# Optimization experiments

Measured on AMD Instinct MI355X. Metric: run time of the kernel, lower is better.

The kernel has to match this reference:

```python
import jax, jax.numpy as jnp
import numpy as np

B, S, D, H = 4, 2048, 2048, 16
HD = D // H  # 128


def setup_inputs() -> dict:
    key = jax.random.key(0)
    k1, k2, k3 = jax.random.split(key, 3)
    sc = 1.0 / np.sqrt(D)
    return {
        "x": jax.random.normal(k1, (B, S, D), dtype=jnp.float32),
        "W_qkv": jax.random.normal(k2, (D, 3 * D), dtype=jnp.float32) * sc,
        "W_out": jax.random.normal(k3, (D, D), dtype=jnp.float32) * sc,
        "b_out": jnp.zeros((D,), dtype=jnp.float32),
    }


def _rotate_half(t):
    t1, t2 = jnp.split(t, 2, axis=-1)
    return jnp.concatenate([-t2, t1], axis=-1)


def reference(x, W_qkv, W_out, b_out):
    b, s, d = x.shape
    qkv = jnp.einsum('bsd,de->bse', x, W_qkv)  # fused QKV projection
    q, k, v = jnp.split(qkv, 3, axis=-1)
    # [b, h, s, hd]
    q = q.reshape(b, s, H, HD).transpose(0, 2, 1, 3)
    k = k.reshape(b, s, H, HD).transpose(0, 2, 1, 3)
    v = v.reshape(b, s, H, HD).transpose(0, 2, 1, 3)
    # RoPE (NeoX-style half-split), past_kv=None so positions = arange(s)
    pos = jnp.arange(s, dtype=jnp.float32)
    theta = 1.0 / (10000.0 ** (jnp.arange(0, HD, 2, dtype=jnp.float32) / HD))
    angles = pos[:, None] * theta[None, :]           # [s, hd/2]
    cos = jnp.concatenate([jnp.cos(angles)] * 2, -1)  # [s, hd] (repeat halves)
    sin = jnp.concatenate([jnp.sin(angles)] * 2, -1)
    cos = cos[None, None]  # [1,1,s,hd]
    sin = sin[None, None]
    q = q * cos + _rotate_half(q) * sin
    k = k * cos + _rotate_half(k) * sin
    # causal SDPA, scale = 1/sqrt(head_dim)
    scale = 1.0 / jnp.sqrt(jnp.asarray(HD, dtype=q.dtype))
    scores = jnp.einsum('bhqd,bhkd->bhqk', q, k) * scale
    causal = jnp.tril(jnp.ones((s, s), dtype=bool))
    scores = jnp.where(causal[None, None], scores, jnp.finfo(scores.dtype).min)
    attn = jax.nn.softmax(scores, axis=-1)
    out = jnp.einsum('bhqk,bhkd->bhqd', attn, v)
    out = out.transpose(0, 2, 1, 3).reshape(b, s, D)
    return jnp.einsum('bsd,de->bse', out, W_out) + b_out
```

## Files before the change

### kernel.cpp

```cpp
#include <hip/hip_runtime.h>

typedef unsigned short ushort_t;
typedef unsigned int u32;
typedef __attribute__((ext_vector_type(8))) short bf16x8;
typedef __attribute__((ext_vector_type(8))) unsigned short u16x8;
typedef __attribute__((ext_vector_type(4))) float f32x4;

#define B_ 4
#define S_ 2048
#define D_ 2048
#define H_ 16
#define HD_ 128

__device__ __forceinline__ ushort_t f2bf(float f) {
  u32 x = __builtin_bit_cast(u32, f);
  x += 0x7fffu + ((x >> 16) & 1u);
  return (ushort_t)(x >> 16);
}
__device__ __forceinline__ float bf2f(ushort_t u) {
  u32 x = ((u32)u) << 16;
  return __builtin_bit_cast(float, x);
}

#define GLL16(srcp, ldsp)                                            \
  __builtin_amdgcn_global_load_lds(                                  \
      (const __attribute__((address_space(1))) u32*)(srcp),          \
      (__attribute__((address_space(3))) u32*)(ldsp), 16, 0, 0)

struct __align__(8) us4 { ushort_t x, y, z, w; };

__global__ void k_cvt_bf16(const float* __restrict__ in, ushort_t* __restrict__ out, int n) {
  int i = (blockIdx.x * 256 + threadIdx.x) * 4;
  if (i >= n) return;
  float4 v = *(const float4*)(in + i);
  us4 o;
  o.x = f2bf(v.x); o.y = f2bf(v.y); o.z = f2bf(v.z); o.w = f2bf(v.w);
  *(us4*)(out + i) = o;
}

__global__ void k_transpose_bf16(const float* __restrict__ in, ushort_t* __restrict__ out,
                                 int R, int C) {
  __shared__ float ld[32][33];
  int c0 = blockIdx.x * 32, r0 = blockIdx.y * 32;
  int tc = threadIdx.x & 31, tr = threadIdx.x >> 5;
#pragma unroll
  for (int i = 0; i < 4; ++i) {
    int r = tr + i * 8;
    ld[r][tc] = in[(size_t)(r0 + r) * C + c0 + tc];
  }
  __syncthreads();
#pragma unroll
  for (int i = 0; i < 4; ++i) {
    int r = tr + i * 8;
    out[(size_t)(c0 + r) * R + r0 + tc] = f2bf(ld[tc][r]);
  }
}

__global__ void k_rope_tables(float* __restrict__ cost, float* __restrict__ sint) {
  int i = blockIdx.x * 256 + threadIdx.x;
  int s = i >> 6, j = i & 63;
  double th = pow(10000.0, -(double)j / 64.0);
  double a = (double)s * th;
  cost[i] = (float)cos(a);
  sint[i] = (float)sin(a);
}

template <int FINAL>
__global__ __launch_bounds__(512) void k_gemm8p(const ushort_t* __restrict__ A,
                                                const ushort_t* __restrict__ Bt,
                                                void* __restrict__ Cout,
                                                const float* __restrict__ bias,
                                                int M, int N, int K) {
  __shared__ __attribute__((aligned(16))) ushort_t As[2][256 * 64];
  __shared__ __attribute__((aligned(16))) ushort_t Bs[2][256 * 64];
  const int tid = threadIdx.x;
  const int w = tid >> 6, l = tid & 63;
  const int lr = l & 15, lg = l >> 4;

  const int cpx = gridDim.x >> 3;
  const int bid = blockIdx.x;
  const int swzid = (bid & 7) * cpx + (bid >> 3);
  const int nbn = N >> 8;
  const size_t m0 = (size_t)(swzid / nbn) * 256;
  const size_t n0 = (size_t)(swzid % nbn) * 256;

  const size_t Kp = (size_t)K * 2;
  const char* Ab = (const char*)A + m0 * Kp;
  const char* Bb = (const char*)Bt + n0 * Kp;

  const int r0 = tid >> 3;
  const int ci16 = (tid & 7) * 16;
  const int sw0 = (((tid & 7) ^ (r0 & 7)) << 4);

#define STG_HALF(gbase, hrow, ldsbase, tcol)                                   \
  {                                                                            \
    GLL16((gbase) + (size_t)((hrow) + r0) * Kp + (tcol) + sw0,                 \
          (char*)(ldsbase) + ((hrow) + r0) * 128 + ci16);                      \
    GLL16((gbase) + (size_t)((hrow) + r0 + 64) * Kp + (tcol) + sw0,            \
          (char*)(ldsbase) + ((hrow) + r0 + 64) * 128 + ci16);                 \
  }

  const int cko0 = (((0 * 4 + lg) ^ (lr & 7)) << 4);
  const int cko1 = (((1 * 4 + lg) ^ (lr & 7)) << 4);

  f32x4 acc[16][2] = {};
  const int NT = K >> 6;

  STG_HALF(Ab, 0, As[0], 0);
  STG_HALF(Bb, 0, Bs[0], 0);
  STG_HALF(Bb, 128, Bs[0], 0);
  STG_HALF(Ab, 128, As[0], 0);
  if (w < 4) asm volatile("s_waitcnt vmcnt(4)");
  else       asm volatile("s_waitcnt vmcnt(2)");
  __builtin_amdgcn_sched_barrier(0);
  __builtin_amdgcn_s_barrier();

  bf16x8 bq[2][2];
  for (int t = 0; t < NT; ++t) {
    const int buf = t & 1;
    const char* Ac = (const char*)As[buf];
    const char* Bc = (const char*)Bs[buf];
    const size_t tc1 = (size_t)(t + 1) * 128;
    const bool more = (t + 1 < NT);
#pragma unroll
    for (int p = 0; p < 4; ++p) {
      if (more) {
        if (p == 0) STG_HALF(Ab, 0, As[buf ^ 1], tc1)
        else if (p == 1) STG_HALF(Bb, 0, Bs[buf ^ 1], tc1)
        else if (p == 2) STG_HALF(Bb, 128, Bs[buf ^ 1], tc1)
        else STG_HALF(Ab, 128, As[buf ^ 1], tc1)
      }
      bf16x8 af[4][2];
#pragma unroll
      for (int m = 0; m < 4; ++m) {
        const int row = p * 64 + m * 16 + lr;
        af[m][0] = *(const bf16x8*)(Ac + row * 128 + cko0);
        af[m][1] = *(const bf16x8*)(Ac + row * 128 + cko1);
      }
      if (p == 0) {
#pragma unroll
        for (int n = 0; n < 2; ++n) {
          const int row = w * 32 + n * 16 + lr;
          bq[n][0] = *(const bf16x8*)(Bc + row * 128 + cko0);
          bq[n][1] = *(const bf16x8*)(Bc + row * 128 + cko1);
        }
      }
      __builtin_amdgcn_s_barrier();
      asm volatile("s_waitcnt lgkmcnt(0)");
      __builtin_amdgcn_sched_barrier(0);
      __builtin_amdgcn_s_setprio(1);
#pragma unroll
      for (int m = 0; m < 4; ++m)
#pragma unroll
        for (int n = 0; n < 2; ++n) {
          acc[p * 4 + m][n] =
              __builtin_amdgcn_mfma_f32_16x16x32_bf16(af[m][0], bq[n][0], acc[p * 4 + m][n], 0, 0, 0);
          acc[p * 4 + m][n] =
              __builtin_amdgcn_mfma_f32_16x16x32_bf16(af[m][1], bq[n][1], acc[p * 4 + m][n], 0, 0, 0);
        }
      __builtin_amdgcn_s_setprio(0);
      if (p == 1) {
        if (more) asm volatile("s_waitcnt vmcnt(4)");
        else      asm volatile("s_waitcnt vmcnt(0)");
        __builtin_amdgcn_sched_barrier(0);
      } else if (p == 3 && more) {
        if (w < 4) asm volatile("s_waitcnt vmcnt(4)");
        else       asm volatile("s_waitcnt vmcnt(2)");
        __builtin_amdgcn_sched_barrier(0);
      }
      __builtin_amdgcn_s_barrier();
    }
  }

#pragma unroll
  for (int n = 0; n < 2; ++n) {
    const size_t col = n0 + w * 32 + n * 16 + lr;
    float bia = FINAL ? bias[col] : 0.f;
#pragma unroll
    for (int mq = 0; mq < 16; ++mq) {
#pragma unroll
      for (int j = 0; j < 4; ++j) {
        const size_t row = m0 + mq * 16 + lg * 4 + j;
        if (FINAL) ((float*)Cout)[row * N + col] = acc[mq][n][j] + bia;
        else       ((ushort_t*)Cout)[row * N + col] = f2bf(acc[mq][n][j]);
      }
    }
  }
#undef STG_HALF
}

__global__ void k_split_rope(const ushort_t* __restrict__ tmp, ushort_t* __restrict__ dst,
                             const float* __restrict__ cost, const float* __restrict__ sint,
                             int mode, float qscale) {
  int s0 = blockIdx.x * 32;
  int h = blockIdx.y;
  int b = blockIdx.z;
  int bh = b * H_ + h;
  if (mode < 2) {
    const int t = threadIdx.x;
    const int sr = t >> 3, dj = (t & 7) * 8;
    const int s = s0 + sr;
    const size_t base = (size_t)(b * S_ + s) * D_ + h * HD_;
    u16x8 lo = *(const u16x8*)(tmp + base + dj);
    u16x8 hi = *(const u16x8*)(tmp + base + 64 + dj);
    const float* cs = cost + s * 64 + dj;
    const float* sn = sint + s * 64 + dj;
    u16x8 olo, ohi;
#pragma unroll
    for (int j = 0; j < 8; ++j) {
      float fl = bf2f(lo[j]), fh = bf2f(hi[j]);
      float c = cs[j], sv = sn[j];
      olo[j] = f2bf((fl * c - fh * sv) * qscale);
      ohi[j] = f2bf((fh * c + fl * sv) * qscale);
    }
    ushort_t* dp = dst + ((size_t)bh * S_ + s) * HD_;
    *(u16x8*)(dp + dj) = olo;
    *(u16x8*)(dp + 64 + dj) = ohi;
  } else {
    __shared__ ushort_t ld[32][132];
#pragma unroll
    for (int i = 0; i < 2; ++i) {
      int e = i * 256 + threadIdx.x;
      int sr = e >> 4, dj = (e & 15) * 8;
      *(u16x8*)&ld[sr][dj] = *(const u16x8*)(tmp + (size_t)(b * S_ + s0 + sr) * D_ + h * HD_ + dj);
    }
    __syncthreads();
#pragma unroll
    for (int i = 0; i < 16; ++i) {
      int e = i * 256 + threadIdx.x;
      int d = e >> 5, sr = e & 31;
      dst[((size_t)bh * HD_ + d) * S_ + s0 + sr] = ld[sr][d];
    }
  }
}

__global__ __launch_bounds__(256, 2) void k_attn4(const ushort_t* __restrict__ Q,
                                                  const ushort_t* __restrict__ K,
                                                  const ushort_t* __restrict__ Vt,
                                                  ushort_t* __restrict__ O) {
  __shared__ __attribute__((aligned(16))) ushort_t Ks[2][64 * 128];
  __shared__ __attribute__((aligned(16))) ushort_t Vs[128 * 64];
  __shared__ __attribute__((aligned(16))) ushort_t Pl[8][16 * 72];

  const int id = blockIdx.x;
  const int work = (id & 7) * 128 + (id >> 3);
  const int bh = work >> 4;
  const int qt = 15 - (work & 15);
  const int b = bh >> 4, h = bh & 15;

  const int tid = threadIdx.x;
  const int w = tid >> 6, l = tid & 63;
  const int lr = l & 15, lg = l >> 4;
  const int qb = qt * 128 + w * 32;

  const ushort_t* Qp = Q + (size_t)bh * S_ * HD_;
  const char* Kpb = (const char*)(K + (size_t)bh * S_ * HD_);
  const char* Vpb = (const char*)(Vt + (size_t)bh * HD_ * S_);

  int kr[4], ksz[4], vr[4], vsz[4];
#pragma unroll
  for (int r = 0; r < 4; ++r) {
    int c = r * 256 + tid;
    kr[r] = c >> 4;
    ksz[r] = (((c & 15) ^ (kr[r] & 15)) << 4);
    vr[r] = c >> 3;
    vsz[r] = (((c & 7) ^ (vr[r] & 7)) << 4);
  }

#define STAGE_K(kb_, bufi)                                                       \
  {                                                                              \
    _Pragma("unroll") for (int r = 0; r < 4; ++r)                                \
        GLL16(Kpb + (size_t)((kb_) + kr[r]) * 256 + ksz[r],                      \
              (char*)Ks[bufi] + (size_t)(r * 256 + tid) * 16);                   \
  }
#define STAGE_V(kb_)                                                             \
  {                                                                              \
    _Pragma("unroll") for (int r = 0; r < 4; ++r)                                \
        GLL16(Vpb + (size_t)vr[r] * (S_ * 2) + (size_t)(kb_) * 2 + vsz[r],       \
              (char*)Vs + (size_t)(r * 256 + tid) * 16);                         \
  }

  bf16x8 qf[2][4];
#pragma unroll
  for (int f = 0; f < 2; ++f)
#pragma unroll
    for (int dw = 0; dw < 4; ++dw)
      qf[f][dw] = *(const bf16x8*)(Qp + (size_t)(qb + f * 16 + lr) * HD_ + dw * 32 + lg * 8);

  f32x4 oacc[2][8] = {};
  float mr[2] = {-1e30f, -1e30f};
  float lsum[2] = {0.f, 0.f};
  const int nkt = 2 * qt + 2;

  STAGE_K(0, 0);
  for (int kt = 0; kt < nkt; ++kt) {
    const int kb = kt * 64;
    const int cur = kt & 1;
    const bool morek = (kt + 1 < nkt);
    if (morek) STAGE_K(kb + 64, cur ^ 1);
    STAGE_V(kb);
    if (morek) asm volatile("s_waitcnt vmcnt(8)");
    else       asm volatile("s_waitcnt vmcnt(4)");
    __builtin_amdgcn_sched_barrier(0);
    __builtin_amdgcn_s_barrier();

    const bool live = (kb <= qb + 31);
    f32x4 st[2][4];
    if (live) {
      const char* Kc = (const char*)Ks[cur];
      __builtin_amdgcn_s_setprio(1);
#pragma unroll
      for (int t = 0; t < 4; ++t) {
        bf16x8 kf[4];
#pragma unroll
        for (int dw = 0; dw < 4; ++dw)
          kf[dw] = *(const bf16x8*)(Kc + (t * 16 + lr) * 256 + (((dw * 4 + lg) ^ lr) << 4));
        f32x4 a0 = {}, a1 = {};
#pragma unroll
        for (int dw = 0; dw < 4; ++dw) {
          a0 = __builtin_amdgcn_mfma_f32_16x16x32_bf16(kf[dw], qf[0][dw], a0, 0, 0, 0);
          a1 = __builtin_amdgcn_mfma_f32_16x16x32_bf16(kf[dw], qf[1][dw], a1, 0, 0, 0);
        }
        st[0][t] = a0;
        st[1][t] = a1;
      }
      __builtin_amdgcn_s_setprio(0);

#pragma unroll
      for (int f = 0; f < 2; ++f) {
        const int qg = qb + f * 16 + lr;
        const bool full = (kb + 63) <= (qb + f * 16);
        float tmax = -1e30f;
        if (full) {
#pragma unroll
          for (int t = 0; t < 4; ++t)
#pragma unroll
            for (int j = 0; j < 4; ++j) tmax = fmaxf(tmax, st[f][t][j]);
        } else {
#pragma unroll
          for (int t = 0; t < 4; ++t)
#pragma unroll
            for (int j = 0; j < 4; ++j) {
              int kg = kb + t * 16 + lg * 4 + j;
              float s = (kg > qg) ? -1e30f : st[f][t][j];
              st[f][t][j] = s;
              tmax = fmaxf(tmax, s);
            }
        }
        tmax = fmaxf(tmax, __shfl_xor(tmax, 16, 64));
        tmax = fmaxf(tmax, __shfl_xor(tmax, 32, 64));
        if (!__all(tmax <= mr[f] + 8.f)) {
          float mnew = fmaxf(mr[f], tmax);
          float alpha = exp2f(mr[f] - mnew);
          mr[f] = mnew;
          lsum[f] *= alpha;
          float a0 = __shfl(alpha, lg * 4 + 0, 64);
          float a1 = __shfl(alpha, lg * 4 + 1, 64);
          float a2 = __shfl(alpha, lg * 4 + 2, 64);
          float a3 = __shfl(alpha, lg * 4 + 3, 64);
#pragma unroll
          for (int dt = 0; dt < 8; ++dt) {
            oacc[f][dt][0] *= a0;
            oacc[f][dt][1] *= a1;
            oacc[f][dt][2] *= a2;
            oacc[f][dt][3] *= a3;
          }
        }
        float psum = 0.f;
        ushort_t* Pw = (ushort_t*)Pl[w * 2 + f];
#pragma unroll
        for (int t = 0; t < 4; ++t) {
          float p0 = exp2f(st[f][t][0] - mr[f]);
          float p1 = exp2f(st[f][t][1] - mr[f]);
          float p2 = exp2f(st[f][t][2] - mr[f]);
          float p3 = exp2f(st[f][t][3] - mr[f]);
          psum += (p0 + p1) + (p2 + p3);
          u32 pk0, pk1;
          asm("v_cvt_pk_bf16_f32 %0, %1, %2" : "=v"(pk0) : "v"(p0), "v"(p1));
          asm("v_cvt_pk_bf16_f32 %0, %1, %2" : "=v"(pk1) : "v"(p2), "v"(p3));
          *(u32*)&Pw[lr * 72 + t * 16 + lg * 4] = pk0;
          *(u32*)&Pw[lr * 72 + t * 16 + lg * 4 + 2] = pk1;
        }
        psum += __shfl_xor(psum, 16, 64);
        psum += __shfl_xor(psum, 32, 64);
        lsum[f] += psum;
      }
    }
    if (morek) asm volatile("s_waitcnt vmcnt(4)");
    else       asm volatile("s_waitcnt vmcnt(0)");
    __builtin_amdgcn_sched_barrier(0);
    __builtin_amdgcn_s_barrier();

    if (live) {
      __builtin_amdgcn_s_setprio(1);
#pragma unroll
      for (int kw = 0; kw < 2; ++kw) {
        bf16x8 pa0 = *(const bf16x8*)&Pl[w * 2 + 0][lr * 72 + kw * 32 + lg * 8];
        bf16x8 pa1 = *(const bf16x8*)&Pl[w * 2 + 1][lr * 72 + kw * 32 + lg * 8];
#pragma unroll
        for (int dt = 0; dt < 8; ++dt) {
          bf16x8 vf = *(const bf16x8*)((const char*)Vs + (dt * 16 + lr) * 128 +
                                       (((kw * 4 + lg) ^ (lr & 7)) << 4));
          oacc[0][dt] = __builtin_amdgcn_mfma_f32_16x16x32_bf16(pa0, vf, oacc[0][dt], 0, 0, 0);
          oacc[1][dt] = __builtin_amdgcn_mfma_f32_16x16x32_bf16(pa1, vf, oacc[1][dt], 0, 0, 0);
        }
      }
      __builtin_amdgcn_s_setprio(0);
    }
    __builtin_amdgcn_s_barrier();
  }

#pragma unroll
  for (int f = 0; f < 2; ++f) {
    float l0 = __shfl(lsum[f], lg * 4 + 0, 64);
    float l1 = __shfl(lsum[f], lg * 4 + 1, 64);
    float l2 = __shfl(lsum[f], lg * 4 + 2, 64);
    float l3 = __shfl(lsum[f], lg * 4 + 3, 64);
    float i0 = 1.f / l0, i1 = 1.f / l1, i2 = 1.f / l2, i3 = 1.f / l3;
    ushort_t* Op = O + (size_t)(b * S_ + qb + f * 16) * D_ + h * HD_;
#pragma unroll
    for (int dt = 0; dt < 8; ++dt) {
      Op[(size_t)(lg * 4 + 0) * D_ + dt * 16 + lr] = f2bf(oacc[f][dt][0] * i0);
      Op[(size_t)(lg * 4 + 1) * D_ + dt * 16 + lr] = f2bf(oacc[f][dt][1] * i1);
      Op[(size_t)(lg * 4 + 2) * D_ + dt * 16 + lr] = f2bf(oacc[f][dt][2] * i2);
      Op[(size_t)(lg * 4 + 3) * D_ + dt * 16 + lr] = f2bf(oacc[f][dt][3] * i3);
    }
  }
#undef STAGE_K
#undef STAGE_V
}

extern "C" void kernel_launch(void* const* d_in, const int* in_sizes, int n_in,
                              void* d_out, int out_size, void* d_ws, size_t ws_size,
                              hipStream_t stream) {
  const float* x = (const float*)d_in[0];
  const float* Wqkv = (const float*)d_in[1];
  const float* Wout = (const float*)d_in[2];
  const float* bout = (const float*)d_in[3];
  char* ws = (char*)d_ws;

  ushort_t* xb = (ushort_t*)(ws + 0);
  ushort_t* Wqt = (ushort_t*)(ws + 33554432ull);
  ushort_t* tmp = (ushort_t*)(ws + 58720256ull);
  ushort_t* Qb = (ushort_t*)(ws + 92274688ull);
  ushort_t* Kb = (ushort_t*)(ws + 125829120ull);
  ushort_t* Vb = (ushort_t*)(ws + 159383552ull);
  float* cost = (float*)(ws + 192937984ull);
  float* sint = (float*)(ws + 193462272ull);

  const int M = B_ * S_;
  const float kSc = 0.08838834764831845f * 1.4426950408889634f;

  k_cvt_bf16<<<dim3((M * D_) / 4 / 256), 256, 0, stream>>>(x, xb, M * D_);
  k_transpose_bf16<<<dim3(3 * D_ / 32, D_ / 32), 256, 0, stream>>>(Wqkv, Wqt, D_, 3 * D_);
  k_rope_tables<<<dim3(S_ * 64 / 256), 256, 0, stream>>>(cost, sint);

  for (int p = 0; p < 3; ++p) {
    k_gemm8p<0><<<dim3((M / 256) * (D_ / 256)), 512, 0, stream>>>(
        xb, Wqt + (size_t)p * D_ * D_, tmp, nullptr, M, D_, D_);
    ushort_t* dst = (p == 0) ? Qb : (p == 1) ? Kb : Vb;
    k_split_rope<<<dim3(S_ / 32, H_, B_), 256, 0, stream>>>(
        tmp, dst, cost, sint, p, (p == 0) ? kSc : 1.0f);
  }

  k_attn4<<<dim3((S_ / 128) * B_ * H_), 256, 0, stream>>>(Qb, Kb, Vb, xb );

  k_transpose_bf16<<<dim3(D_ / 32, D_ / 32), 256, 0, stream>>>(Wout, tmp, D_, D_);
  k_gemm8p<1><<<dim3((M / 256) * (D_ / 256)), 512, 0, stream>>>(
      xb, tmp, d_out, bout, M, D_, D_);
}
```

Measured before the change: 554.4 us.

## Fuse QKV GEMMs, scatter heads in epilogue, restructure GEMM warps and attention V loads

The three per-projection GEMMs become one fused QKV GEMM whose epilogue writes straight into per-head [b,h,s,d] layout, so the separate split kernel and the tmp round trip go away. RoPE now runs in place, and V gets its own transpose kernel. The GEMM moves to a 2x4 warp grid with 128x64 warp tiles, different load staging and fewer barriers, at 2 blocks per CU. Attention drops the LDS staging of V in favour of direct global loads, swizzles the P buffer and raises occupancy to 3 blocks. The risks are register pressure and uncoalesced global V reads.

```diff
diff --git a/kernel.cpp b/kernel.cpp
--- a/kernel.cpp
+++ b/kernel.cpp
@@ -65,17 +65,21 @@
   sint[i] = (float)sin(a);
 }
 
-template <int FINAL>
-__global__ __launch_bounds__(512) void k_gemm8p(const ushort_t* __restrict__ A,
-                                                const ushort_t* __restrict__ Bt,
-                                                void* __restrict__ Cout,
-                                                const float* __restrict__ bias,
-                                                int M, int N, int K) {
+template <int MODE>
+__global__ __launch_bounds__(512, 2) void k_gemm8w(const ushort_t* __restrict__ A,
+                                                   const ushort_t* __restrict__ Bt,
+                                                   void* __restrict__ Cout,
+                                                   const float* __restrict__ bias,
+                                                   int M, int N, int K) {
   __shared__ __attribute__((aligned(16))) ushort_t As[2][256 * 64];
   __shared__ __attribute__((aligned(16))) ushort_t Bs[2][256 * 64];
   const int tid = threadIdx.x;
   const int w = tid >> 6, l = tid & 63;
   const int lr = l & 15, lg = l >> 4;
+  const int wm = w >> 2, wn = w & 3;
+  const int ga = w & 3;
+  const int hbB = wn >> 1;
+  const int rbB = (w & 1) | ((w >> 1) & 2);
 
   const int cpx = gridDim.x >> 3;
   const int bid = blockIdx.x;
@@ -88,164 +92,196 @@
   const char* Ab = (const char*)A + m0 * Kp;
   const char* Bb = (const char*)Bt + n0 * Kp;
 
-  const int r0 = tid >> 3;
-  const int ci16 = (tid & 7) * 16;
-  const int sw0 = (((tid & 7) ^ (r0 & 7)) << 4);
-
-#define STG_HALF(gbase, hrow, ldsbase, tcol)                                   \
-  {                                                                            \
-    GLL16((gbase) + (size_t)((hrow) + r0) * Kp + (tcol) + sw0,                 \
-          (char*)(ldsbase) + ((hrow) + r0) * 128 + ci16);                      \
-    GLL16((gbase) + (size_t)((hrow) + r0 + 64) * Kp + (tcol) + sw0,            \
-          (char*)(ldsbase) + ((hrow) + r0 + 64) * 128 + ci16);                 \
-  }
-
-  const int cko0 = (((0 * 4 + lg) ^ (lr & 7)) << 4);
-  const int cko1 = (((1 * 4 + lg) ^ (lr & 7)) << 4);
-
-  f32x4 acc[16][2] = {};
+  int arow[4], acs[4], adst[4], brow[4], bcs[4], bdst[4];
+#pragma unroll
+  for (int j = 0; j < 4; ++j) {
+    int c = j * 64 + l;
+    int ra = wm * 128 + ga * 32 + (c >> 3);
+    arow[j] = ra;
+    acs[j] = ((c & 7) ^ (ra & 7)) << 4;
+    adst[j] = ra * 128 + ((c & 7) << 4);
+    int rb = hbB * 128 + rbB * 32 + (c >> 3);
+    brow[j] = rb;
+    bcs[j] = ((c & 7) ^ (rb & 7)) << 4;
+    bdst[j] = rb * 128 + ((c & 7) << 4);
+  }
+
+#define STG_A(colb, bufi)                                                  \
+  { _Pragma("unroll") for (int j = 0; j < 4; ++j)                          \
+      GLL16(Ab + (size_t)arow[j] * Kp + (colb) + acs[j],                   \
+            (char*)As[bufi] + adst[j]); }
+#define STG_B(colb, bufi)                                                  \
+  { _Pragma("unroll") for (int j = 0; j < 4; ++j)                          \
+      GLL16(Bb + (size_t)brow[j] * Kp + (colb) + bcs[j],                   \
+            (char*)Bs[bufi] + bdst[j]); }
+
+  f32x4 acc[8][4] = {};
   const int NT = K >> 6;
 
-  STG_HALF(Ab, 0, As[0], 0);
-  STG_HALF(Bb, 0, Bs[0], 0);
-  STG_HALF(Bb, 128, Bs[0], 0);
-  STG_HALF(Ab, 128, As[0], 0);
-  if (w < 4) asm volatile("s_waitcnt vmcnt(4)");
-  else       asm volatile("s_waitcnt vmcnt(2)");
-  __builtin_amdgcn_sched_barrier(0);
-  __builtin_amdgcn_s_barrier();
-
-  bf16x8 bq[2][2];
+  STG_B((size_t)0, 0);
+  STG_A((size_t)0, 0);
+
   for (int t = 0; t < NT; ++t) {
     const int buf = t & 1;
     const char* Ac = (const char*)As[buf];
     const char* Bc = (const char*)Bs[buf];
-    const size_t tc1 = (size_t)(t + 1) * 128;
     const bool more = (t + 1 < NT);
+    const size_t tcol = (size_t)(t + 1) * 128;
+    bf16x8 bq[4][2];
 #pragma unroll
     for (int p = 0; p < 4; ++p) {
-      if (more) {
-        if (p == 0) STG_HALF(Ab, 0, As[buf ^ 1], tc1)
-        else if (p == 1) STG_HALF(Bb, 0, Bs[buf ^ 1], tc1)
-        else if (p == 2) STG_HALF(Bb, 128, Bs[buf ^ 1], tc1)
-        else STG_HALF(Ab, 128, As[buf ^ 1], tc1)
-      }
-      bf16x8 af[4][2];
-#pragma unroll
-      for (int m = 0; m < 4; ++m) {
-        const int row = p * 64 + m * 16 + lr;
-        af[m][0] = *(const bf16x8*)(Ac + row * 128 + cko0);
-        af[m][1] = *(const bf16x8*)(Ac + row * 128 + cko1);
-      }
       if (p == 0) {
-#pragma unroll
-        for (int n = 0; n < 2; ++n) {
-          const int row = w * 32 + n * 16 + lr;
-          bq[n][0] = *(const bf16x8*)(Bc + row * 128 + cko0);
-          bq[n][1] = *(const bf16x8*)(Bc + row * 128 + cko1);
+        if (ga == 0) asm volatile("s_waitcnt vmcnt(0)");
+        else         asm volatile("s_waitcnt vmcnt(4)");
+        __builtin_amdgcn_sched_barrier(0);
+      } else if (p == 1) {
+        if (ga == 1) {
+          if (more) asm volatile("s_waitcnt vmcnt(4)");
+          else      asm volatile("s_waitcnt vmcnt(0)");
+          __builtin_amdgcn_sched_barrier(0);
+        }
+      } else if (p == 2) {
+        if (ga == 2) {
+          if (more) asm volatile("s_waitcnt vmcnt(4)");
+          else      asm volatile("s_waitcnt vmcnt(0)");
+          __builtin_amdgcn_sched_barrier(0);
+        }
+      } else {
+        if (ga == 3) {
+          if (more) asm volatile("s_waitcnt vmcnt(8)");
+          else      asm volatile("s_waitcnt vmcnt(0)");
+          __builtin_amdgcn_sched_barrier(0);
         }
       }
       __builtin_amdgcn_s_barrier();
+      if (p == 0 && more) {
+        STG_B(tcol, buf ^ 1);
+        if (ga == 0) STG_A(tcol, buf ^ 1);
+      }
+      if (p == 2 && more && ga != 0) STG_A(tcol, buf ^ 1);
+      bf16x8 af[2][2];
+#pragma unroll
+      for (int m2 = 0; m2 < 2; ++m2) {
+        const int row = wm * 128 + (p * 2 + m2) * 16 + lr;
+#pragma unroll
+        for (int k2 = 0; k2 < 2; ++k2)
+          af[m2][k2] = *(const bf16x8*)(Ac + row * 128 + (((k2 * 4 + lg) ^ (lr & 7)) << 4));
+      }
+      if (p == 0) {
+#pragma unroll
+        for (int n = 0; n < 4; ++n) {
+          const int row = wn * 64 + n * 16 + lr;
+#pragma unroll
+          for (int k2 = 0; k2 < 2; ++k2)
+            bq[n][k2] = *(const bf16x8*)(Bc + row * 128 + (((k2 * 4 + lg) ^ (lr & 7)) << 4));
+        }
+      }
       asm volatile("s_waitcnt lgkmcnt(0)");
       __builtin_amdgcn_sched_barrier(0);
       __builtin_amdgcn_s_setprio(1);
 #pragma unroll
-      for (int m = 0; m < 4; ++m)
-#pragma unroll
-        for (int n = 0; n < 2; ++n) {
-          acc[p * 4 + m][n] =
-              __builtin_amdgcn_mfma_f32_16x16x32_bf16(af[m][0], bq[n][0], acc[p * 4 + m][n], 0, 0, 0);
-          acc[p * 4 + m][n] =
-              __builtin_amdgcn_mfma_f32_16x16x32_bf16(af[m][1], bq[n][1], acc[p * 4 + m][n], 0, 0, 0);
+      for (int m2 = 0; m2 < 2; ++m2)
+#pragma unroll
+        for (int n = 0; n < 4; ++n) {
+          acc[p * 2 + m2][n] =
+              __builtin_amdgcn_mfma_f32_16x16x32_bf16(af[m2][0], bq[n][0], acc[p * 2 + m2][n], 0, 0, 0);
+          acc[p * 2 + m2][n] =
+              __builtin_amdgcn_mfma_f32_16x16x32_bf16(af[m2][1], bq[n][1], acc[p * 2 + m2][n], 0, 0, 0);
         }
       __builtin_amdgcn_s_setprio(0);
-      if (p == 1) {
-        if (more) asm volatile("s_waitcnt vmcnt(4)");
-        else      asm volatile("s_waitcnt vmcnt(0)");
-        __builtin_amdgcn_sched_barrier(0);
-      } else if (p == 3 && more) {
-        if (w < 4) asm volatile("s_waitcnt vmcnt(4)");
-        else       asm volatile("s_waitcnt vmcnt(2)");
-        __builtin_amdgcn_sched_barrier(0);
-      }
-      __builtin_amdgcn_s_barrier();
     }
   }
 
-#pragma unroll
-  for (int n = 0; n < 2; ++n) {
-    const size_t col = n0 + w * 32 + n * 16 + lr;
-    float bia = FINAL ? bias[col] : 0.f;
-#pragma unroll
-    for (int mq = 0; mq < 16; ++mq) {
-#pragma unroll
-      for (int j = 0; j < 4; ++j) {
-        const size_t row = m0 + mq * 16 + lg * 4 + j;
-        if (FINAL) ((float*)Cout)[row * N + col] = acc[mq][n][j] + bia;
-        else       ((ushort_t*)Cout)[row * N + col] = f2bf(acc[mq][n][j]);
-      }
+  if (MODE == 2) {
+#pragma unroll
+    for (int n = 0; n < 4; ++n) {
+      const size_t col = n0 + wn * 64 + n * 16 + lr;
+      const float bia = bias[col];
+#pragma unroll
+      for (int m = 0; m < 8; ++m)
+#pragma unroll
+        for (int j = 0; j < 4; ++j) {
+          const size_t row = m0 + wm * 128 + m * 16 + lg * 4 + j;
+          ((float*)Cout)[row * N + col] = acc[m][n][j] + bia;
+        }
     }
-  }
-#undef STG_HALF
-}
-
-__global__ void k_split_rope(const ushort_t* __restrict__ tmp, ushort_t* __restrict__ dst,
-                             const float* __restrict__ cost, const float* __restrict__ sint,
-                             int mode, float qscale) {
-  int s0 = blockIdx.x * 32;
-  int h = blockIdx.y;
-  int b = blockIdx.z;
+  } else {
+    ushort_t* Qbase = (ushort_t*)Cout;
+#pragma unroll
+    for (int n = 0; n < 4; ++n) {
+      const int col = (int)n0 + wn * 64 + n * 16 + lr;
+      const int p3 = col >> 11, rem = col & 2047;
+      const int h = rem >> 7, d = rem & 127;
+      ushort_t* base = Qbase + (size_t)p3 * 16777216ull + (size_t)h * (S_ * HD_) + d;
+#pragma unroll
+      for (int m = 0; m < 8; ++m)
+#pragma unroll
+        for (int j = 0; j < 4; ++j) {
+          const int row = (int)m0 + wm * 128 + m * 16 + lg * 4 + j;
+          const int b2 = row >> 11, s = row & 2047;
+          base[(size_t)b2 * (H_ * S_ * HD_) + (size_t)s * HD_] = f2bf(acc[m][n][j]);
+        }
+    }
+  }
+#undef STG_A
+#undef STG_B
+}
+
+__global__ void k_rope2(ushort_t* __restrict__ t8, const float* __restrict__ cost,
+                        const float* __restrict__ sint, float qscale) {
+  int s0 = blockIdx.x * 32, h = blockIdx.y, b = blockIdx.z;
   int bh = b * H_ + h;
-  if (mode < 2) {
-    const int t = threadIdx.x;
-    const int sr = t >> 3, dj = (t & 7) * 8;
-    const int s = s0 + sr;
-    const size_t base = (size_t)(b * S_ + s) * D_ + h * HD_;
-    u16x8 lo = *(const u16x8*)(tmp + base + dj);
-    u16x8 hi = *(const u16x8*)(tmp + base + 64 + dj);
-    const float* cs = cost + s * 64 + dj;
-    const float* sn = sint + s * 64 + dj;
-    u16x8 olo, ohi;
-#pragma unroll
-    for (int j = 0; j < 8; ++j) {
-      float fl = bf2f(lo[j]), fh = bf2f(hi[j]);
-      float c = cs[j], sv = sn[j];
-      olo[j] = f2bf((fl * c - fh * sv) * qscale);
-      ohi[j] = f2bf((fh * c + fl * sv) * qscale);
-    }
-    ushort_t* dp = dst + ((size_t)bh * S_ + s) * HD_;
-    *(u16x8*)(dp + dj) = olo;
-    *(u16x8*)(dp + 64 + dj) = ohi;
-  } else {
-    __shared__ ushort_t ld[32][132];
-#pragma unroll
-    for (int i = 0; i < 2; ++i) {
-      int e = i * 256 + threadIdx.x;
-      int sr = e >> 4, dj = (e & 15) * 8;
-      *(u16x8*)&ld[sr][dj] = *(const u16x8*)(tmp + (size_t)(b * S_ + s0 + sr) * D_ + h * HD_ + dj);
-    }
-    __syncthreads();
-#pragma unroll
-    for (int i = 0; i < 16; ++i) {
-      int e = i * 256 + threadIdx.x;
-      int d = e >> 5, sr = e & 31;
-      dst[((size_t)bh * HD_ + d) * S_ + s0 + sr] = ld[sr][d];
-    }
-  }
-}
-
-__global__ __launch_bounds__(256, 2) void k_attn4(const ushort_t* __restrict__ Q,
+  const int t = threadIdx.x;
+  const int sr = t >> 3, dj = (t & 7) * 8;
+  const int s = s0 + sr;
+  ushort_t* base = t8 + ((size_t)bh * S_ + s) * HD_;
+  u16x8 lo = *(const u16x8*)(base + dj);
+  u16x8 hi = *(const u16x8*)(base + 64 + dj);
+  const float* cs = cost + s * 64 + dj;
+  const float* sn = sint + s * 64 + dj;
+  u16x8 olo, ohi;
+#pragma unroll
+  for (int j = 0; j < 8; ++j) {
+    float fl = bf2f(lo[j]), fh = bf2f(hi[j]);
+    float c = cs[j], sv = sn[j];
+    olo[j] = f2bf((fl * c - fh * sv) * qscale);
+    ohi[j] = f2bf((fh * c + fl * sv) * qscale);
+  }
+  *(u16x8*)(base + dj) = olo;
+  *(u16x8*)(base + 64 + dj) = ohi;
+}
+
+__global__ void k_transT(const ushort_t* __restrict__ src, ushort_t* __restrict__ dst) {
+  __shared__ ushort_t ld[32][33];
+  int s0 = blockIdx.x * 32, d0 = blockIdx.y * 32, bh = blockIdx.z;
+  const ushort_t* S = src + (size_t)bh * S_ * HD_;
+  ushort_t* D = dst + (size_t)bh * HD_ * S_;
+  const int tid = threadIdx.x;
+#pragma unroll
+  for (int i = 0; i < 4; ++i) {
+    int e = i * 256 + tid;
+    int sr = e >> 5, dc = e & 31;
+    ld[sr][dc] = S[(size_t)(s0 + sr) * HD_ + d0 + dc];
+  }
+  __syncthreads();
+#pragma unroll
+  for (int i = 0; i < 4; ++i) {
+    int e = i * 256 + tid;
+    int dc = e >> 5, sr = e & 31;
+    D[(size_t)(d0 + dc) * S_ + s0 + sr] = ld[sr][dc];
+  }
+}
+
+__global__ __launch_bounds__(256, 3) void k_attn5(const ushort_t* __restrict__ Q,
                                                   const ushort_t* __restrict__ K,
                                                   const ushort_t* __restrict__ Vt,
                                                   ushort_t* __restrict__ O) {
   __shared__ __attribute__((aligned(16))) ushort_t Ks[2][64 * 128];
-  __shared__ __attribute__((aligned(16))) ushort_t Vs[128 * 64];
-  __shared__ __attribute__((aligned(16))) ushort_t Pl[8][16 * 72];
+  __shared__ __attribute__((aligned(16))) ushort_t Pl[8][1024];
 
   const int id = blockIdx.x;
-  const int work = (id & 7) * 128 + (id >> 3);
-  const int bh = work >> 4;
-  const int qt = 15 - (work & 15);
+  const int qt = 15 - (id >> 6);
+  const int bh = id & 63;
   const int b = bh >> 4, h = bh & 15;
 
   const int tid = threadIdx.x;
@@ -257,28 +293,20 @@
   const char* Kpb = (const char*)(K + (size_t)bh * S_ * HD_);
   const char* Vpb = (const char*)(Vt + (size_t)bh * HD_ * S_);
 
-  int kr[4], ksz[4], vr[4], vsz[4];
+  int kr[4], ksz[4];
 #pragma unroll
   for (int r = 0; r < 4; ++r) {
     int c = r * 256 + tid;
     kr[r] = c >> 4;
-    ksz[r] = (((c & 15) ^ (kr[r] & 15)) << 4);
-    vr[r] = c >> 3;
-    vsz[r] = (((c & 7) ^ (vr[r] & 7)) << 4);
+    ksz[r] = ((c & 15) ^ (kr[r] & 15)) << 4;
   }
 
 #define STAGE_K(kb_, bufi)                                                       \
-  {                                                                              \
-    _Pragma("unroll") for (int r = 0; r < 4; ++r)                                \
-        GLL16(Kpb + (size_t)((kb_) + kr[r]) * 256 + ksz[r],                      \
-              (char*)Ks[bufi] + (size_t)(r * 256 + tid) * 16);                   \
-  }
-#define STAGE_V(kb_)                                                             \
-  {                                                                              \
-    _Pragma("unroll") for (int r = 0; r < 4; ++r)                                \
-        GLL16(Vpb + (size_t)vr[r] * (S_ * 2) + (size_t)(kb_) * 2 + vsz[r],       \
-              (char*)Vs + (size_t)(r * 256 + tid) * 16);                         \
-  }
+  { _Pragma("unroll") for (int r = 0; r < 4; ++r)                                \
+      GLL16(Kpb + (size_t)((kb_) + kr[r]) * 256 + ksz[r],                        \
+            (char*)Ks[bufi] + (size_t)(r * 256 + tid) * 16); }
+
+  STAGE_K(0, 0);
 
   bf16x8 qf[2][4];
 #pragma unroll
@@ -292,22 +320,23 @@
   float lsum[2] = {0.f, 0.f};
   const int nkt = 2 * qt + 2;
 
-  STAGE_K(0, 0);
   for (int kt = 0; kt < nkt; ++kt) {
     const int kb = kt * 64;
     const int cur = kt & 1;
     const bool morek = (kt + 1 < nkt);
-    if (morek) STAGE_K(kb + 64, cur ^ 1);
-    STAGE_V(kb);
-    if (morek) asm volatile("s_waitcnt vmcnt(8)");
-    else       asm volatile("s_waitcnt vmcnt(4)");
+    if (morek) {
+      STAGE_K(kb + 64, cur ^ 1);
+      asm volatile("s_waitcnt vmcnt(4)");
+    } else {
+      asm volatile("s_waitcnt vmcnt(0)");
+    }
     __builtin_amdgcn_sched_barrier(0);
     __builtin_amdgcn_s_barrier();
 
     const bool live = (kb <= qb + 31);
-    f32x4 st[2][4];
     if (live) {
       const char* Kc = (const char*)Ks[cur];
+      f32x4 st[2][4];
       __builtin_amdgcn_s_setprio(1);
 #pragma unroll
       for (int t = 0; t < 4; ++t) {
@@ -367,7 +396,7 @@
           }
         }
         float psum = 0.f;
-        ushort_t* Pw = (ushort_t*)Pl[w * 2 + f];
+        char* Pw = (char*)Pl + (w * 2 + f) * 2048;
 #pragma unroll
         for (int t = 0; t < 4; ++t) {
           float p0 = exp2f(st[f][t][0] - mr[f]);
@@ -378,34 +407,35 @@
           u32 pk0, pk1;
           asm("v_cvt_pk_bf16_f32 %0, %1, %2" : "=v"(pk0) : "v"(p0), "v"(p1));
           asm("v_cvt_pk_bf16_f32 %0, %1, %2" : "=v"(pk1) : "v"(p2), "v"(p3));
-          *(u32*)&Pw[lr * 72 + t * 16 + lg * 4] = pk0;
-          *(u32*)&Pw[lr * 72 + t * 16 + lg * 4 + 2] = pk1;
+          const int byt = lr * 128 + (((2 * t + (lg >> 1)) ^ (lr & 7)) << 4) + ((lg & 1) << 3);
+          *(u32*)(Pw + byt) = pk0;
+          *(u32*)(Pw + byt + 4) = pk1;
         }
         psum += __shfl_xor(psum, 16, 64);
         psum += __shfl_xor(psum, 32, 64);
         lsum[f] += psum;
       }
-    }
-    if (morek) asm volatile("s_waitcnt vmcnt(4)");
-    else       asm volatile("s_waitcnt vmcnt(0)");
-    __builtin_amdgcn_sched_barrier(0);
-    __builtin_amdgcn_s_barrier();
-
-    if (live) {
-      __builtin_amdgcn_s_setprio(1);
+
+      const char* Pw0 = (const char*)Pl + (w * 2) * 2048;
+      const char* Pw1 = (const char*)Pl + (w * 2 + 1) * 2048;
 #pragma unroll
       for (int kw = 0; kw < 2; ++kw) {
-        bf16x8 pa0 = *(const bf16x8*)&Pl[w * 2 + 0][lr * 72 + kw * 32 + lg * 8];
-        bf16x8 pa1 = *(const bf16x8*)&Pl[w * 2 + 1][lr * 72 + kw * 32 + lg * 8];
+        bf16x8 vf[8];
+#pragma unroll
+        for (int dt = 0; dt < 8; ++dt)
+          vf[dt] = *(const bf16x8*)(Vpb + ((size_t)(dt * 16 + lr) * S_ + kb + kw * 32 + lg * 8) * 2);
+        const int pbyt = lr * 128 + (((kw * 4 + lg) ^ (lr & 7)) << 4);
+        bf16x8 pa0 = *(const bf16x8*)(Pw0 + pbyt);
+        bf16x8 pa1 = *(const bf16x8*)(Pw1 + pbyt);
+        __builtin_amdgcn_s_setprio(1);
 #pragma unroll
         for (int dt = 0; dt < 8; ++dt) {
-          bf16x8 vf = *(const bf16x8*)((const char*)Vs + (dt * 16 + lr) * 128 +
-                                       (((kw * 4 + lg) ^ (lr & 7)) << 4));
-          oacc[0][dt] = __builtin_amdgcn_mfma_f32_16x16x32_bf16(pa0, vf, oacc[0][dt], 0, 0, 0);
-          oacc[1][dt] = __builtin_amdgcn_mfma_f32_16x16x32_bf16(pa1, vf, oacc[1][dt], 0, 0, 0);
-        }
-      }
-      __builtin_amdgcn_s_setprio(0);
+          oacc[0][dt] = __builtin_amdgcn_mfma_f32_16x16x32_bf16(pa0, vf[dt], oacc[0][dt], 0, 0, 0);
+          oacc[1][dt] = __builtin_amdgcn_mfma_f32_16x16x32_bf16(pa1, vf[dt], oacc[1][dt], 0, 0, 0);
+        }
+        __builtin_amdgcn_s_setprio(0);
+        __builtin_amdgcn_sched_barrier(0);
+      }
     }
     __builtin_amdgcn_s_barrier();
   }
@@ -427,7 +457,6 @@
     }
   }
 #undef STAGE_K
-#undef STAGE_V
 }
 
 extern "C" void kernel_launch(void* const* d_in, const int* in_sizes, int n_in,
@@ -439,14 +468,14 @@
   const float* bout = (const float*)d_in[3];
   char* ws = (char*)d_ws;
 
-  ushort_t* xb = (ushort_t*)(ws + 0);
+  ushort_t* xb  = (ushort_t*)(ws + 0);
   ushort_t* Wqt = (ushort_t*)(ws + 33554432ull);
-  ushort_t* tmp = (ushort_t*)(ws + 58720256ull);
-  ushort_t* Qb = (ushort_t*)(ws + 92274688ull);
-  ushort_t* Kb = (ushort_t*)(ws + 125829120ull);
-  ushort_t* Vb = (ushort_t*)(ws + 159383552ull);
-  float* cost = (float*)(ws + 192937984ull);
-  float* sint = (float*)(ws + 193462272ull);
+  ushort_t* Qr  = (ushort_t*)(ws + 58720256ull);
+  ushort_t* Kr  = (ushort_t*)(ws + 92274688ull);
+  ushort_t* Vr  = (ushort_t*)(ws + 125829120ull);
+  ushort_t* Vt  = (ushort_t*)(ws + 159383552ull);
+  float* cost   = (float*)(ws + 192937984ull);
+  float* sint   = (float*)(ws + 193462272ull);
 
   const int M = B_ * S_;
   const float kSc = 0.08838834764831845f * 1.4426950408889634f;
@@ -455,17 +484,17 @@
   k_transpose_bf16<<<dim3(3 * D_ / 32, D_ / 32), 256, 0, stream>>>(Wqkv, Wqt, D_, 3 * D_);
   k_rope_tables<<<dim3(S_ * 64 / 256), 256, 0, stream>>>(cost, sint);
 
-  for (int p = 0; p < 3; ++p) {
-    k_gemm8p<0><<<dim3((M / 256) * (D_ / 256)), 512, 0, stream>>>(
-        xb, Wqt + (size_t)p * D_ * D_, tmp, nullptr, M, D_, D_);
-    ushort_t* dst = (p == 0) ? Qb : (p == 1) ? Kb : Vb;
-    k_split_rope<<<dim3(S_ / 32, H_, B_), 256, 0, stream>>>(
-        tmp, dst, cost, sint, p, (p == 0) ? kSc : 1.0f);
-  }
-
-  k_attn4<<<dim3((S_ / 128) * B_ * H_), 256, 0, stream>>>(Qb, Kb, Vb, xb );
-
-  k_transpose_bf16<<<dim3(D_ / 32, D_ / 32), 256, 0, stream>>>(Wout, tmp, D_, D_);
-  k_gemm8p<1><<<dim3((M / 256) * (D_ / 256)), 512, 0, stream>>>(
-      xb, tmp, d_out, bout, M, D_, D_);
-}
+  k_gemm8w<1><<<dim3((M / 256) * (3 * D_ / 256)), 512, 0, stream>>>(
+      xb, Wqt, Qr, nullptr, M, 3 * D_, D_);
+
+  k_rope2<<<dim3(S_ / 32, H_, B_), 256, 0, stream>>>(Qr, cost, sint, kSc);
+  k_rope2<<<dim3(S_ / 32, H_, B_), 256, 0, stream>>>(Kr, cost, sint, 1.0f);
+  k_transT<<<dim3(S_ / 32, HD_ / 32, B_ * H_), 256, 0, stream>>>(Vr, Vt);
+
+  k_transpose_bf16<<<dim3(D_ / 32, D_ / 32), 256, 0, stream>>>(Wout, Vr, D_, D_);
+
+  k_attn5<<<dim3((S_ / 128) * B_ * H_), 256, 0, stream>>>(Qr, Kr, Vt, xb );
+
+  k_gemm8w<2><<<dim3((M / 256) * (D_ / 256)), 512, 0, stream>>>(
+      xb, Vr, d_out, bout, M, D_, D_);
+}
```

Result: slower. 740.3 us (+33.5%).
